# Optimization experiments

Hardware: AMD Instinct MI355X
Metric: run time of the kernel (lower is better)

## Reference

```python
import jax, jax.numpy as jnp
import numpy as np

N, E = 50000, 800000
D_IN, D_HID, D_OUT = 128, 64, 32
NEG_SLOPE = 0.2


def _gat_layer(h_in, src, dst, W, a_s, a_d, b):
    # h_in: [N, din], W: [din, dout]
    h = h_in @ W                                   # [N, dout]
    alpha_src = h @ a_s                            # [N]
    alpha_dst = h @ a_d                            # [N]
    e = jax.nn.leaky_relu(alpha_src[src] + alpha_dst[dst], NEG_SLOPE)  # [E']
    # segment softmax over incoming edges of each dst node
    m = jax.ops.segment_max(e, dst, num_segments=N)
    ex = jnp.exp(e - m[dst])
    s = jax.ops.segment_sum(ex, dst, num_segments=N)
    w = ex / s[dst]                                # [E']
    out = jax.ops.segment_sum(h[src] * w[:, None], dst, num_segments=N)
    return out + b


def setup_inputs() -> dict:
    key = jax.random.key(0)
    ks = jax.random.split(key, 16)
    x = jax.random.normal(ks[0], (N, D_IN), dtype=jnp.float32)
    edge_index = jax.random.randint(ks[1], (2, E), 0, N, dtype=jnp.int64)
    dims = [(D_IN, D_HID), (D_HID, D_HID), (D_HID, D_OUT)]
    inp = {"x": x, "edge_index": edge_index}
    for i, (din, dout) in enumerate(dims):
        sc = 1.0 / np.sqrt(din)
        inp[f"W{i}"] = jax.random.normal(ks[2 + 4 * i], (din, dout), dtype=jnp.float32) * sc
        inp[f"as{i}"] = jax.random.normal(ks[3 + 4 * i], (dout,), dtype=jnp.float32) * 0.1
        inp[f"ad{i}"] = jax.random.normal(ks[4 + 4 * i], (dout,), dtype=jnp.float32) * 0.1
        inp[f"b{i}"] = jnp.zeros((dout,), dtype=jnp.float32)
    return inp


def reference(x, edge_index, W0, as0, ad0, b0, W1, as1, ad1, b1, W2, as2, ad2, b2):
    # add self loops (PyG GATConv default)
    loop = jnp.arange(N, dtype=edge_index.dtype)
    src = jnp.concatenate([edge_index[0], loop])
    dst = jnp.concatenate([edge_index[1], loop])
    h = jax.nn.relu(_gat_layer(x, src, dst, W0, as0, ad0, b0))
    h = jax.nn.relu(_gat_layer(h, src, dst, W1, as1, ad1, b1))
    h = jnp.tanh(_gat_layer(h, src, dst, W2, as2, ad2, b2))
    return h
```

## Files before the change

### kernel.cpp

```cpp
#include <hip/hip_runtime.h>
#include <hip/hip_fp16.h>
#include <math.h>

#define N_NODES 50000
#define E_EDGES 800000
#define ETOT    (E_EDGES + N_NODES)

#define BUCK_SHIFT 9
#define BUCK_SZ   (1 << BUCK_SHIFT)
#define NBUCK ((N_NODES + BUCK_SZ - 1) >> BUCK_SHIFT)
#define BS_EPT 16
#define BS_THREADS 256
#define BS_EPB (BS_THREADS * BS_EPT)
#define BS_NBLK ((ETOT + BS_EPB - 1) / BS_EPB)

#define GEMM0_GRID ((N_NODES + 63) / 64)
#define PACK_GRID (GEMM0_GRID + BS_NBLK)

__global__ __launch_bounds__(BS_THREADS)
void hist_kernel(const int* __restrict__ ei, int* __restrict__ bcnt)
{
    __shared__ int lcnt[NBUCK];
    const int t = threadIdx.x;
    for (int i = t; i < NBUCK; i += BS_THREADS) lcnt[i] = 0;
    __syncthreads();
    const int e0 = blockIdx.x * BS_EPB;
#pragma unroll
    for (int k = 0; k < BS_EPT; ++k) {
        const int eid = e0 + k * BS_THREADS + t;
        if (eid < ETOT) {
            int dst = (eid < E_EDGES) ? ei[E_EDGES + eid] : (eid - E_EDGES);
            atomicAdd(&lcnt[dst >> BUCK_SHIFT], 1);
        }
    }
    __syncthreads();
    for (int i = t; i < NBUCK; i += BS_THREADS)
        if (lcnt[i] > 0) atomicAdd(&bcnt[i], lcnt[i]);
}

__global__ __launch_bounds__(256)
void gemm0_binscatter_kernel(const float* __restrict__ X,
                             const float* __restrict__ W,
                             const float* __restrict__ a_s,
                             const float* __restrict__ a_d,
                             __half* __restrict__ H16,
                             float* __restrict__ asrc,
                             float* __restrict__ adst,
                             const int* __restrict__ ei,
                             const int* __restrict__ bcnt,
                             int* __restrict__ cur,
                             unsigned int* __restrict__ tmp)
{
    __shared__ float smem[128 * 64];
    const int t = threadIdx.x;

    if (blockIdx.x < GEMM0_GRID) {
        constexpr int DIN = 128, DOUT = 64, COLG = 16;
        float* Wl = smem;
        for (int i = t; i < DIN * DOUT / 4; i += 256)
            ((float4*)Wl)[i] = ((const float4*)W)[i];
        __syncthreads();

        const int row0b = blockIdx.x * 64;
        const int tx = t % COLG;
        const int ty = t / COLG;
        const int r0 = ty * 4;
        const int c0 = tx * 4;

        const float* Xr[4];
#pragma unroll
        for (int i = 0; i < 4; ++i) {
            int gr = row0b + r0 + i;
            Xr[i] = X + (size_t)min(gr, N_NODES - 1) * DIN;
        }

        float acc[4][4] = {};
#pragma unroll 4
        for (int kk = 0; kk < DIN; kk += 4) {
            float a[4][4], w[4][4];
#pragma unroll
            for (int i = 0; i < 4; ++i)
                *(float4*)a[i] = *(const float4*)&Xr[i][kk];
#pragma unroll
            for (int j = 0; j < 4; ++j)
                *(float4*)w[j] = *(const float4*)&Wl[(kk + j) * DOUT + c0];
#pragma unroll
            for (int i = 0; i < 4; ++i)
#pragma unroll
                for (int j = 0; j < 4; ++j)
                    acc[i][j] = fmaf(a[i][0], w[0][j],
                                fmaf(a[i][1], w[1][j],
                                fmaf(a[i][2], w[2][j],
                                fmaf(a[i][3], w[3][j], acc[i][j]))));
        }

        float as4[4], ad4[4];
        *(float4*)as4 = *(const float4*)&a_s[c0];
        *(float4*)ad4 = *(const float4*)&a_d[c0];

#pragma unroll
        for (int i = 0; i < 4; ++i) {
            const int gr = row0b + r0 + i;
            float ps = acc[i][0] * as4[0] + acc[i][1] * as4[1] +
                       acc[i][2] * as4[2] + acc[i][3] * as4[3];
            float pd = acc[i][0] * ad4[0] + acc[i][1] * ad4[1] +
                       acc[i][2] * ad4[2] + acc[i][3] * ad4[3];
#pragma unroll
            for (int off = COLG / 2; off >= 1; off >>= 1) {
                ps += __shfl_xor(ps, off, 64);
                pd += __shfl_xor(pd, off, 64);
            }
            if (gr < N_NODES) {
                __half2 p01 = __floats2half2_rn(acc[i][0], acc[i][1]);
                __half2 p23 = __floats2half2_rn(acc[i][2], acc[i][3]);
                uint2 pk;
                pk.x = *(unsigned int*)&p01;
                pk.y = *(unsigned int*)&p23;
                *(uint2*)&H16[gr * DOUT + c0] = pk;
                if (tx == 0) { asrc[gr] = ps; adst[gr] = pd; }
            }
        }
    } else {
        int* lcnt  = (int*)smem;
        int* lbase = lcnt + 128;
        int* lscan = lbase + 128;

        const int v = (t < NBUCK) ? bcnt[t] : 0;
        lscan[t] = v;
        __syncthreads();
        for (int off = 1; off < 256; off <<= 1) {
            int u = (t >= off) ? lscan[t - off] : 0;
            __syncthreads();
            lscan[t] += u;
            __syncthreads();
        }
        if (t < NBUCK) lbase[t] = lscan[t] - v;
        for (int i = t; i < NBUCK; i += 256) lcnt[i] = 0;
        __syncthreads();

        const int e0 = (blockIdx.x - GEMM0_GRID) * BS_EPB;
        unsigned int pk[BS_EPT];
        int rk[BS_EPT];
        int bk[BS_EPT];
#pragma unroll
        for (int k = 0; k < BS_EPT; ++k) {
            const int eid = e0 + k * BS_THREADS + t;
            bk[k] = -1;
            if (eid < ETOT) {
                int src, dst;
                if (eid < E_EDGES) { src = ei[eid]; dst = ei[E_EDGES + eid]; }
                else               { src = dst = eid - E_EDGES; }
                bk[k] = dst >> BUCK_SHIFT;
                pk[k] = ((unsigned int)dst << 16) | (unsigned int)src;
                rk[k] = atomicAdd(&lcnt[bk[k]], 1);
            }
        }
        __syncthreads();
        for (int i = t; i < NBUCK; i += 256)
            if (lcnt[i] > 0) lbase[i] += atomicAdd(&cur[i], lcnt[i]);
        __syncthreads();
#pragma unroll
        for (int k = 0; k < BS_EPT; ++k)
            if (bk[k] >= 0) tmp[lbase[bk[k]] + rk[k]] = pk[k];
    }
}

__global__ __launch_bounds__(BUCK_SZ)
void bucket_sort_kernel(const unsigned int* __restrict__ tmp,
                        const int* __restrict__ bcnt,
                        unsigned int* __restrict__ csr_pk,
                        int* __restrict__ offs)
{
    __shared__ int lcnt[BUCK_SZ];
    __shared__ int loff[BUCK_SZ];
    __shared__ int lcur[BUCK_SZ];
    __shared__ int sbase;
    const int bk = blockIdx.x;
    const int t  = threadIdx.x;

    {
        const int v = (t < NBUCK) ? bcnt[t] : 0;
        lcnt[t] = v;
        __syncthreads();
        for (int off = 1; off < 128; off <<= 1) {
            int u = (t >= off && t < 128) ? lcnt[t - off] : 0;
            __syncthreads();
            if (t < 128) lcnt[t] += u;
            __syncthreads();
        }
        if (t == bk) sbase = lcnt[t] - v;
    }
    __syncthreads();
    const int base = sbase;
    const int cnt  = bcnt[bk];

    lcnt[t] = 0;
    __syncthreads();
    for (int i = t; i < cnt; i += BUCK_SZ)
        atomicAdd(&lcnt[(tmp[base + i] >> 16) & (BUCK_SZ - 1)], 1);
    __syncthreads();

    const int v = lcnt[t];
    loff[t] = v;
    __syncthreads();
    for (int off = 1; off < BUCK_SZ; off <<= 1) {
        int u = (t >= off) ? loff[t - off] : 0;
        __syncthreads();
        loff[t] += u;
        __syncthreads();
    }
    const int excl = loff[t] - v;

    const int g = (bk << BUCK_SHIFT) + t;
    if (g <= N_NODES) offs[g] = base + excl;

    lcur[t] = excl;
    __syncthreads();
    for (int i = t; i < cnt; i += BUCK_SZ) {
        const unsigned int pk = tmp[base + i];
        const int l = (pk >> 16) & (BUCK_SZ - 1);
        const int pos = atomicAdd(&lcur[l], 1);
        csr_pk[base + pos] = pk;
    }
}

template<int DIN, int DOUT>
__global__ __launch_bounds__(256)
void gemm_alpha_kernel(const float* __restrict__ X, const float* __restrict__ W,
                       const float* __restrict__ a_s, const float* __restrict__ a_d,
                       __half* __restrict__ H16, float* __restrict__ asrc,
                       float* __restrict__ adst)
{
    constexpr int COLG = DOUT / 4;
    constexpr int ROWG = 256 / COLG;
    constexpr int BM   = ROWG * 4;

    __shared__ float Wl[DIN * DOUT];

    const int tid = threadIdx.x;
    const int row0b = blockIdx.x * BM;

    for (int i = tid; i < DIN * DOUT / 4; i += 256)
        ((float4*)Wl)[i] = ((const float4*)W)[i];
    __syncthreads();

    const int tx = tid % COLG;
    const int ty = tid / COLG;
    const int r0 = ty * 4;
    const int c0 = tx * 4;

    const float* Xr[4];
#pragma unroll
    for (int i = 0; i < 4; ++i) {
        int gr = row0b + r0 + i;
        Xr[i] = X + (size_t)min(gr, N_NODES - 1) * DIN;
    }

    float acc[4][4] = {};
#pragma unroll 4
    for (int kk = 0; kk < DIN; kk += 4) {
        float a[4][4], w[4][4];
#pragma unroll
        for (int i = 0; i < 4; ++i)
            *(float4*)a[i] = *(const float4*)&Xr[i][kk];
#pragma unroll
        for (int j = 0; j < 4; ++j)
            *(float4*)w[j] = *(const float4*)&Wl[(kk + j) * DOUT + c0];
#pragma unroll
        for (int i = 0; i < 4; ++i)
#pragma unroll
            for (int j = 0; j < 4; ++j)
                acc[i][j] = fmaf(a[i][0], w[0][j],
                            fmaf(a[i][1], w[1][j],
                            fmaf(a[i][2], w[2][j],
                            fmaf(a[i][3], w[3][j], acc[i][j]))));
    }

    float as4[4], ad4[4];
    *(float4*)as4 = *(const float4*)&a_s[c0];
    *(float4*)ad4 = *(const float4*)&a_d[c0];

#pragma unroll
    for (int i = 0; i < 4; ++i) {
        const int gr = row0b + r0 + i;
        float ps = acc[i][0] * as4[0] + acc[i][1] * as4[1] +
                   acc[i][2] * as4[2] + acc[i][3] * as4[3];
        float pd = acc[i][0] * ad4[0] + acc[i][1] * ad4[1] +
                   acc[i][2] * ad4[2] + acc[i][3] * ad4[3];
#pragma unroll
        for (int off = COLG / 2; off >= 1; off >>= 1) {
            ps += __shfl_xor(ps, off, 64);
            pd += __shfl_xor(pd, off, 64);
        }
        if (gr < N_NODES) {
            __half2 p01 = __floats2half2_rn(acc[i][0], acc[i][1]);
            __half2 p23 = __floats2half2_rn(acc[i][2], acc[i][3]);
            uint2 pk;
            pk.x = *(unsigned int*)&p01;
            pk.y = *(unsigned int*)&p23;
            *(uint2*)&H16[gr * DOUT + c0] = pk;
            if (tx == 0) { asrc[gr] = ps; adst[gr] = pd; }
        }
    }
}

template<int DOUT, int ACT>
__global__ __launch_bounds__(256)
void node_agg_kernel(const int* __restrict__ offs,
                     const unsigned int* __restrict__ csr_pk,
                     const float* __restrict__ asrc,
                     const float* __restrict__ adst,
                     const __half* __restrict__ H16,
                     const float* __restrict__ b,
                     float* __restrict__ out)
{
    constexpr int FL    = DOUT / 8;
    constexpr int SLOTS = 64 / FL;
    const int wv   = threadIdx.x >> 6;
    const int lane = threadIdx.x & 63;
    const int fl   = lane % FL;
    const int slot = lane / FL;
    const int node = blockIdx.x * 4 + wv;
    if (node >= N_NODES) return;

    const int beg = offs[node];
    const int end = offs[node + 1];
    const float adn = adst[node];
    const __half* __restrict__ Hf = H16 + fl * 8;

    float s = 0.f;
    float acc[8] = {};

    int eid = beg + slot;
    bool valid = (eid < end);
    unsigned int pk = valid ? csr_pk[eid] : 0u;

    for (int cb = beg; cb < end; cb += SLOTS) {
        const int nid = cb + SLOTS + slot;
        const bool nvalid = (nid < end);
        const unsigned int npk = nvalid ? csr_pk[nid] : 0u;

        float p = 0.f;
        uint4 h = make_uint4(0u, 0u, 0u, 0u);
        if (valid) {
            const unsigned int src = pk & 0xffffu;
            float v = asrc[src] + adn;
            v = fmaxf(v, 0.2f * v);
            p = __expf(fminf(v, 80.f));
            h = *(const uint4*)(Hf + src * DOUT);
        }
        const float2 f0 = __half22float2(*(const __half2*)&h.x);
        const float2 f1 = __half22float2(*(const __half2*)&h.y);
        const float2 f2 = __half22float2(*(const __half2*)&h.z);
        const float2 f3 = __half22float2(*(const __half2*)&h.w);
        s += p;
        acc[0] = fmaf(p, f0.x, acc[0]);
        acc[1] = fmaf(p, f0.y, acc[1]);
        acc[2] = fmaf(p, f1.x, acc[2]);
        acc[3] = fmaf(p, f1.y, acc[3]);
        acc[4] = fmaf(p, f2.x, acc[4]);
        acc[5] = fmaf(p, f2.y, acc[5]);
        acc[6] = fmaf(p, f3.x, acc[6]);
        acc[7] = fmaf(p, f3.y, acc[7]);
        valid = nvalid;
        pk = npk;
    }

#pragma unroll
    for (int off = FL; off < 64; off <<= 1) {
        s += __shfl_xor(s, off, 64);
#pragma unroll
        for (int j = 0; j < 8; ++j)
            acc[j] += __shfl_xor(acc[j], off, 64);
    }

    if (slot == 0) {
        const float inv = 1.f / s;
        float o[8];
#pragma unroll
        for (int j = 0; j < 8; ++j) {
            float v = acc[j] * inv + b[fl * 8 + j];
            o[j] = (ACT == 0) ? fmaxf(v, 0.f) : tanhf(v);
        }
        *(float4*)&out[node * DOUT + fl * 8]     = *(float4*)&o[0];
        *(float4*)&out[node * DOUT + fl * 8 + 4] = *(float4*)&o[4];
    }
}


extern "C" void kernel_launch(void* const* d_in, const int* in_sizes, int n_in,
                              void* d_out, int out_size, void* d_ws, size_t ws_size,
                              hipStream_t stream)
{
    const float* x  = (const float*)d_in[0];
    const int*   ei = (const int*)d_in[1];
    const float* W0 = (const float*)d_in[2];
    const float* as0= (const float*)d_in[3];
    const float* ad0= (const float*)d_in[4];
    const float* b0 = (const float*)d_in[5];
    const float* W1 = (const float*)d_in[6];
    const float* as1= (const float*)d_in[7];
    const float* ad1= (const float*)d_in[8];
    const float* b1 = (const float*)d_in[9];
    const float* W2 = (const float*)d_in[10];
    const float* as2= (const float*)d_in[11];
    const float* ad2= (const float*)d_in[12];
    const float* b2 = (const float*)d_in[13];
    float* out = (float*)d_out;

    char* wsb = (char*)d_ws;
    auto take = [&](size_t bytes) {
        char* p = wsb;
        wsb += (bytes + 255) & ~size_t(255);
        return p;
    };
    __half* h16    = (__half*)take(sizeof(__half) * N_NODES * 64);
    float* buf_act = (float*)take(sizeof(float) * N_NODES * 64);
    float* asrc    = (float*)take(sizeof(float) * N_NODES);
    float* adst    = (float*)take(sizeof(float) * N_NODES);
    int*   offs    = (int*)take(sizeof(int) * (N_NODES + 1));
    int*   bc      = (int*)take(sizeof(int) * NBUCK * 2);
    int*   bcnt    = bc;
    int*   cur     = bc + NBUCK;
    unsigned int* tmp    = (unsigned int*)take(sizeof(unsigned int) * ETOT);
    unsigned int* csr_pk = (unsigned int*)take(sizeof(unsigned int) * ETOT);

    hipMemsetAsync(bc, 0, sizeof(int) * NBUCK * 2, stream);

    hist_kernel<<<BS_NBLK, BS_THREADS, 0, stream>>>(ei, bcnt);

    gemm0_binscatter_kernel<<<PACK_GRID, 256, 0, stream>>>(
        x, W0, as0, ad0, h16, asrc, adst, ei, bcnt, cur, tmp);

    bucket_sort_kernel<<<NBUCK, BUCK_SZ, 0, stream>>>(tmp, bcnt, csr_pk, offs);

    const int agg_grid = (N_NODES + 3) / 4;
    node_agg_kernel<64, 0><<<agg_grid, 256, 0, stream>>>(
        offs, csr_pk, asrc, adst, h16, b0, buf_act);

    gemm_alpha_kernel<64, 64><<<GEMM0_GRID, 256, 0, stream>>>(
        buf_act, W1, as1, ad1, h16, asrc, adst);
    node_agg_kernel<64, 0><<<agg_grid, 256, 0, stream>>>(
        offs, csr_pk, asrc, adst, h16, b1, buf_act);

    gemm_alpha_kernel<64, 32><<<(N_NODES + 127) / 128, 256, 0, stream>>>(
        buf_act, W2, as2, ad2, h16, asrc, adst);
    node_agg_kernel<32, 1><<<agg_grid, 256, 0, stream>>>(
        offs, csr_pk, asrc, adst, h16, b2, out);
}
```

Before: 172.5 us.

## Drop histogram pass by scattering into fixed-capacity per-bucket regions

Removes the separate destination-bucket histogram kernel and its prefix scan in the scatter blocks. Each bucket now gets a fixed region of 16384 slots in the temporary buffer, and the atomic cursor doubles as the bucket count, which the bucket sort then scans for CSR offsets. This saves one full read of the destination indices and a kernel launch. In exchange it uses a larger temporary buffer and silently overflows if any bucket receives more than the fixed capacity, which assumes a fairly uniform degree distribution.

```diff
diff --git a/kernel.cpp b/kernel.cpp
--- a/kernel.cpp
+++ b/kernel.cpp
@@ -14,29 +14,11 @@
 #define BS_EPB (BS_THREADS * BS_EPT)
 #define BS_NBLK ((ETOT + BS_EPB - 1) / BS_EPB)
 
+#define CAP_SHIFT 14
+#define CAP (1 << CAP_SHIFT)
+
 #define GEMM0_GRID ((N_NODES + 63) / 64)
 #define PACK_GRID (GEMM0_GRID + BS_NBLK)
-
-__global__ __launch_bounds__(BS_THREADS)
-void hist_kernel(const int* __restrict__ ei, int* __restrict__ bcnt)
-{
-    __shared__ int lcnt[NBUCK];
-    const int t = threadIdx.x;
-    for (int i = t; i < NBUCK; i += BS_THREADS) lcnt[i] = 0;
-    __syncthreads();
-    const int e0 = blockIdx.x * BS_EPB;
-#pragma unroll
-    for (int k = 0; k < BS_EPT; ++k) {
-        const int eid = e0 + k * BS_THREADS + t;
-        if (eid < ETOT) {
-            int dst = (eid < E_EDGES) ? ei[E_EDGES + eid] : (eid - E_EDGES);
-            atomicAdd(&lcnt[dst >> BUCK_SHIFT], 1);
-        }
-    }
-    __syncthreads();
-    for (int i = t; i < NBUCK; i += BS_THREADS)
-        if (lcnt[i] > 0) atomicAdd(&bcnt[i], lcnt[i]);
-}
 
 __global__ __launch_bounds__(256)
 void gemm0_binscatter_kernel(const float* __restrict__ X,
@@ -47,7 +29,6 @@
                              float* __restrict__ asrc,
                              float* __restrict__ adst,
                              const int* __restrict__ ei,
-                             const int* __restrict__ bcnt,
                              int* __restrict__ cur,
                              unsigned int* __restrict__ tmp)
 {
@@ -123,18 +104,7 @@
     } else {
         int* lcnt  = (int*)smem;
         int* lbase = lcnt + 128;
-        int* lscan = lbase + 128;
-
-        const int v = (t < NBUCK) ? bcnt[t] : 0;
-        lscan[t] = v;
-        __syncthreads();
-        for (int off = 1; off < 256; off <<= 1) {
-            int u = (t >= off) ? lscan[t - off] : 0;
-            __syncthreads();
-            lscan[t] += u;
-            __syncthreads();
-        }
-        if (t < NBUCK) lbase[t] = lscan[t] - v;
+
         for (int i = t; i < NBUCK; i += 256) lcnt[i] = 0;
         __syncthreads();
 
@@ -157,7 +127,8 @@
         }
         __syncthreads();
         for (int i = t; i < NBUCK; i += 256)
-            if (lcnt[i] > 0) lbase[i] += atomicAdd(&cur[i], lcnt[i]);
+            if (lcnt[i] > 0)
+                lbase[i] = (i << CAP_SHIFT) + atomicAdd(&cur[i], lcnt[i]);
         __syncthreads();
 #pragma unroll
         for (int k = 0; k < BS_EPT; ++k)
@@ -167,7 +138,7 @@
 
 __global__ __launch_bounds__(BUCK_SZ)
 void bucket_sort_kernel(const unsigned int* __restrict__ tmp,
-                        const int* __restrict__ bcnt,
+                        const int* __restrict__ cur,
                         unsigned int* __restrict__ csr_pk,
                         int* __restrict__ offs)
 {
@@ -179,7 +150,7 @@
     const int t  = threadIdx.x;
 
     {
-        const int v = (t < NBUCK) ? bcnt[t] : 0;
+        const int v = (t < NBUCK) ? cur[t] : 0;
         lcnt[t] = v;
         __syncthreads();
         for (int off = 1; off < 128; off <<= 1) {
@@ -191,13 +162,14 @@
         if (t == bk) sbase = lcnt[t] - v;
     }
     __syncthreads();
-    const int base = sbase;
-    const int cnt  = bcnt[bk];
+    const int base  = sbase;
+    const int tbase = bk << CAP_SHIFT;
+    const int cnt   = cur[bk];
 
     lcnt[t] = 0;
     __syncthreads();
     for (int i = t; i < cnt; i += BUCK_SZ)
-        atomicAdd(&lcnt[(tmp[base + i] >> 16) & (BUCK_SZ - 1)], 1);
+        atomicAdd(&lcnt[(tmp[tbase + i] >> 16) & (BUCK_SZ - 1)], 1);
     __syncthreads();
 
     const int v = lcnt[t];
@@ -217,7 +189,7 @@
     lcur[t] = excl;
     __syncthreads();
     for (int i = t; i < cnt; i += BUCK_SZ) {
-        const unsigned int pk = tmp[base + i];
+        const unsigned int pk = tmp[tbase + i];
         const int l = (pk >> 16) & (BUCK_SZ - 1);
         const int pos = atomicAdd(&lcur[l], 1);
         csr_pk[base + pos] = pk;
@@ -419,20 +391,16 @@
     float* asrc    = (float*)take(sizeof(float) * N_NODES);
     float* adst    = (float*)take(sizeof(float) * N_NODES);
     int*   offs    = (int*)take(sizeof(int) * (N_NODES + 1));
-    int*   bc      = (int*)take(sizeof(int) * NBUCK * 2);
-    int*   bcnt    = bc;
-    int*   cur     = bc + NBUCK;
-    unsigned int* tmp    = (unsigned int*)take(sizeof(unsigned int) * ETOT);
+    int*   cur     = (int*)take(sizeof(int) * NBUCK);
+    unsigned int* tmp    = (unsigned int*)take(sizeof(unsigned int) * NBUCK * CAP);
     unsigned int* csr_pk = (unsigned int*)take(sizeof(unsigned int) * ETOT);
 
-    hipMemsetAsync(bc, 0, sizeof(int) * NBUCK * 2, stream);
-
-    hist_kernel<<<BS_NBLK, BS_THREADS, 0, stream>>>(ei, bcnt);
+    hipMemsetAsync(cur, 0, sizeof(int) * NBUCK, stream);
 
     gemm0_binscatter_kernel<<<PACK_GRID, 256, 0, stream>>>(
-        x, W0, as0, ad0, h16, asrc, adst, ei, bcnt, cur, tmp);
-
-    bucket_sort_kernel<<<NBUCK, BUCK_SZ, 0, stream>>>(tmp, bcnt, csr_pk, offs);
+        x, W0, as0, ad0, h16, asrc, adst, ei, cur, tmp);
+
+    bucket_sort_kernel<<<NBUCK, BUCK_SZ, 0, stream>>>(tmp, cur, csr_pk, offs);
 
     const int agg_grid = (N_NODES + 3) / 4;
     node_agg_kernel<64, 0><<<agg_grid, 256, 0, stream>>>(
```

Measured after the change: 163.7 us, median of 2. 1.05x faster.
